# Kernel optimization log

Measured on AMD Instinct MI355X. Metric: run time of the kernel, lower is better.

## Reference

```python
import jax, jax.numpy as jnp
import numpy as np

N_NODES = 100000
N_EDGES = 1600000
F_IN = 128
HIDDEN = 64
N_CLASSES = 32


def setup_inputs() -> dict:
    key = jax.random.key(0)
    k1, k2, k3, k4 = jax.random.split(key, 4)
    x = jax.random.normal(k1, (N_NODES, F_IN), dtype=jnp.float32)
    edge_index = jax.random.randint(k2, (2, N_EDGES), 0, N_NODES, dtype=jnp.int32)
    # Glorot-style init for the two GCNConv weight matrices
    W1 = jax.random.normal(k3, (F_IN, HIDDEN), dtype=jnp.float32) * (1.0 / np.sqrt(F_IN))
    W2 = jax.random.normal(k4, (HIDDEN, N_CLASSES), dtype=jnp.float32) * (1.0 / np.sqrt(HIDDEN))
    b1 = jnp.zeros((HIDDEN,), dtype=jnp.float32)
    b2 = jnp.zeros((N_CLASSES,), dtype=jnp.float32)
    return {"x": x, "edge_index": edge_index, "W1": W1, "b1": b1, "W2": W2, "b2": b2}


def gcn_conv(x, W, b, src, dst, num_nodes):
    # PyG GCNConv: linear transform first, then normalized neighbor aggregation.
    h = x @ W  # [N, out]
    ones = jnp.ones(src.shape, dtype=h.dtype)
    deg = jax.ops.segment_sum(ones, dst, num_segments=num_nodes)  # in-degree incl. self-loops
    d_inv_sqrt = jnp.where(deg > 0, jax.lax.rsqrt(deg), 0.0)
    norm = d_inv_sqrt[src] * d_inv_sqrt[dst]  # [E]
    msg = h[src] * norm[:, None]              # gather + scale, [E, out]
    out = jax.ops.segment_sum(msg, dst, num_segments=num_nodes)  # scatter-add
    return out + b


def reference(x, edge_index, W1, b1, W2, b2):
    n = x.shape[0]
    # add_self_loops=True (GCNConv default)
    loop = jnp.arange(n, dtype=edge_index.dtype)
    src = jnp.concatenate([edge_index[0], loop])
    dst = jnp.concatenate([edge_index[1], loop])
    h = jax.nn.relu(gcn_conv(x, W1, b1, src, dst, n))
    # F.dropout(training=self.training) is identity in eval mode
    logits = gcn_conv(h, W2, b2, src, dst, n)
    return jax.nn.log_softmax(logits, axis=1)
```

## Files before the change

### kernel.cpp

```cpp
#include <hip/hip_runtime.h>

#define F_IN 128
#define HID 64
#define CLS 32
#define BCAP 8192

typedef short v8s __attribute__((ext_vector_type(8)));
typedef float f4 __attribute__((ext_vector_type(4)));
typedef float f2 __attribute__((ext_vector_type(2)));

__device__ __forceinline__ float bflo(unsigned int w) { return __uint_as_float(w << 16); }
__device__ __forceinline__ float bfhi(unsigned int w) { return __uint_as_float(w & 0xFFFF0000u); }
__device__ __forceinline__ unsigned short f2bf(float f) {
    unsigned int u = __float_as_uint(f);
    u += 0x7FFFu + ((u >> 16) & 1u);
    return (unsigned short)(u >> 16);
}
__device__ __forceinline__ unsigned int pack2(float lo, float hi) {
    return (unsigned int)f2bf(lo) | ((unsigned int)f2bf(hi) << 16);
}
__device__ __forceinline__ unsigned int relu2(unsigned int w) {
    unsigned int lo = (w & 0x8000u) ? 0u : (w & 0xFFFFu);
    unsigned int hi = (w & 0x80000000u) ? 0u : (w & 0xFFFF0000u);
    return lo | hi;
}
__device__ __forceinline__ unsigned char f2fp8(float v) {
    return (unsigned char)(__builtin_amdgcn_cvt_pk_fp8_f32(v, v, 0, false) & 0xFF);
}

__global__ __launch_bounds__(512) void k_init(int* __restrict__ bCursor, int nb) {
    int i = threadIdx.x;
    if (i < nb) bCursor[i] = i * BCAP;
}

__global__ __launch_bounds__(256) void k_bscatter(const int* __restrict__ src,
                                                  const int* __restrict__ dst,
                                                  int* __restrict__ bCursor,
                                                  int* __restrict__ bucketed, int E, int nb) {
    __shared__ int h[512];
    __shared__ int chunk[512];
    int tid = threadIdx.x;
    for (int i = tid; i < nb; i += 256) h[i] = 0;
    __syncthreads();

    int e0 = blockIdx.x * 2048;
    int myRec[8], myB[8], myRank[8];
#pragma unroll
    for (int k = 0; k < 8; ++k) {
        int e = e0 + k * 256 + tid;
        if (e < E) {
            int d = dst[e];
            myB[k] = d >> 8;
            myRec[k] = src[e] | ((d & 255) << 17);
            myRank[k] = atomicAdd(&h[myB[k]], 1);
        } else {
            myB[k] = -1;
        }
    }
    __syncthreads();
    for (int i = tid; i < nb; i += 256)
        chunk[i] = h[i] ? atomicAdd(&bCursor[i], h[i]) : 0;
    __syncthreads();
#pragma unroll
    for (int k = 0; k < 8; ++k) {
        if (myB[k] >= 0) bucketed[chunk[myB[k]] + myRank[k]] = myRec[k];
    }
}

__global__ __launch_bounds__(512) void k_csr(const int* __restrict__ bCursor,
                                             const int* __restrict__ bucketed,
                                             int* __restrict__ pk,
                                             float* __restrict__ dinv, int* __restrict__ csr,
                                             int n) {
    __shared__ int cnt[256];
    __shared__ int s[256];
    __shared__ int cur[256];
    int b = blockIdx.x;
    int node0 = b << 8;
    int tid = threadIdx.x;
    if (tid < 256) cnt[tid] = 0;
    __syncthreads();
    int p0 = b * BCAP, p1 = bCursor[b];
    for (int p = p0 + tid; p < p1; p += 512) {
        int rec = bucketed[p];
        atomicAdd(&cnt[rec >> 17], 1);
    }
    __syncthreads();
    int v = 0;
    if (tid < 256) { v = cnt[tid]; s[tid] = v; }
    __syncthreads();
    for (int off = 1; off < 256; off <<= 1) {
        int t = (tid >= off && tid < 256) ? s[tid - off] : 0;
        __syncthreads();
        if (tid < 256) s[tid] += t;
        __syncthreads();
    }
    if (tid < 256) {
        int myoff = p0 + s[tid] - v;
        cur[tid] = myoff;
        int node = node0 + tid;
        if (node < n) {
            pk[node] = myoff | (v << 22);
            dinv[node] = rsqrtf((float)(v + 1));
        }
    }
    __syncthreads();
    for (int p = p0 + tid; p < p1; p += 512) {
        int rec = bucketed[p];
        int q = atomicAdd(&cur[rec >> 17], 1);
        csr[q] = rec & 0x1FFFF;
    }
}

__global__ __launch_bounds__(256) void k_gemm1(const float* __restrict__ x,
                                               const float* __restrict__ W,
                                               const float* __restrict__ dinv,
                                               unsigned char* __restrict__ y, int n) {
    __shared__ unsigned short Wt[HID * 136];
    int tid = threadIdx.x;
    for (int i = tid; i < F_IN * HID; i += 256) {
        int k = i >> 6, nn = i & 63;
        Wt[nn * 136 + k] = f2bf(W[i]);
    }
    __syncthreads();

    int lane = tid & 63;
    int quad = lane >> 4, c = lane & 15;
    int nstripes = (n + 15) >> 4;
    int stripe = blockIdx.x * 4 + (tid >> 6);
    if (stripe >= nstripes) return;
    int row0 = stripe << 4;

    f4 acc[4] = {};
    union { unsigned int u[4]; v8s v; } au;

#pragma unroll
    for (int ks = 0; ks < 4; ++ks) {
        int k0 = ks * 32 + quad * 8;
        int row = row0 + c;
        if (row >= n) row = n - 1;
        const float* xp = x + (size_t)row * F_IN + k0;
        float4 lo = *(const float4*)xp;
        float4 hi = *(const float4*)(xp + 4);
        au.u[0] = pack2(lo.x, lo.y);
        au.u[1] = pack2(lo.z, lo.w);
        au.u[2] = pack2(hi.x, hi.y);
        au.u[3] = pack2(hi.z, hi.w);
        v8s a = au.v;
#pragma unroll
        for (int nt = 0; nt < 4; ++nt) {
            v8s b = *(const v8s*)&Wt[(nt * 16 + c) * 136 + k0];
            acc[nt] = __builtin_amdgcn_mfma_f32_16x16x32_bf16(a, b, acc[nt], 0, 0, 0);
        }
    }

#pragma unroll
    for (int reg = 0; reg < 4; ++reg) {
        int row = row0 + quad * 4 + reg;
        if (row < n) {
            float dd = dinv[row];
#pragma unroll
            for (int nt = 0; nt < 4; ++nt)
                y[(size_t)row * HID + nt * 16 + c] = f2fp8(acc[nt][reg] * dd);
        }
    }
}

__global__ __launch_bounds__(256) void k_gemm2(const unsigned short* __restrict__ hb,
                                               const float* __restrict__ W,
                                               const float* __restrict__ dinv,
                                               unsigned short* __restrict__ y, int n) {
    __shared__ unsigned short Wt[CLS * 72];
    int tid = threadIdx.x;
    for (int i = tid; i < HID * CLS; i += 256) {
        int k = i >> 5, nn = i & 31;
        Wt[nn * 72 + k] = f2bf(W[i]);
    }
    __syncthreads();

    int lane = tid & 63;
    int quad = lane >> 4, c = lane & 15;
    int nstripes = (n + 15) >> 4;
    int stripe = blockIdx.x * 4 + (tid >> 6);
    if (stripe >= nstripes) return;
    int row0 = stripe << 4;

    f4 acc[2] = {};
    union { unsigned int u[4]; v8s v; } au;

#pragma unroll
    for (int ks = 0; ks < 2; ++ks) {
        int k0 = ks * 32 + quad * 8;
        int row = row0 + c;
        if (row >= n) row = n - 1;
        uint4 w = *(const uint4*)(hb + (size_t)row * HID + k0);
        au.u[0] = relu2(w.x);
        au.u[1] = relu2(w.y);
        au.u[2] = relu2(w.z);
        au.u[3] = relu2(w.w);
        v8s a = au.v;
#pragma unroll
        for (int nt = 0; nt < 2; ++nt) {
            v8s b = *(const v8s*)&Wt[(nt * 16 + c) * 72 + k0];
            acc[nt] = __builtin_amdgcn_mfma_f32_16x16x32_bf16(a, b, acc[nt], 0, 0, 0);
        }
    }

#pragma unroll
    for (int reg = 0; reg < 4; ++reg) {
        int row = row0 + quad * 4 + reg;
        if (row < n) {
            float dd = dinv[row];
#pragma unroll
            for (int nt = 0; nt < 2; ++nt)
                y[(size_t)row * CLS + nt * 16 + c] = f2bf(acc[nt][reg] * dd);
        }
    }
}

__global__ __launch_bounds__(256) void k_gather64(const int* __restrict__ pk,
                                                  const int* __restrict__ csr,
                                                  const unsigned char* __restrict__ xw8,
                                                  const float* __restrict__ b,
                                                  unsigned short* __restrict__ hb, int n) {
    int node = blockIdx.x * 16 + (threadIdx.x >> 4);
    if (node >= n) return;
    int l = threadIdx.x & 15;
    unsigned int pv = (unsigned int)pk[node];
    int p0 = pv & 0x3FFFFF;
    int cntv = (int)(pv >> 22);
    int p1 = p0 + cntv;
    float dd = rsqrtf((float)(cntv + 1));
    unsigned int sw = *(const unsigned int*)(xw8 + (size_t)node * HID + l * 4);

    f2 A0 = {0.f, 0.f}, A1 = A0, B0 = A0, B1 = A0, C0 = A0, C1 = A0, D0 = A0, D1 = A0;
    int p = p0;
    for (; p + 3 < p1; p += 4) {
        int s0 = csr[p], s1 = csr[p + 1], s2 = csr[p + 2], s3 = csr[p + 3];
        unsigned int w0 = *(const unsigned int*)(xw8 + (size_t)s0 * HID + l * 4);
        unsigned int w1 = *(const unsigned int*)(xw8 + (size_t)s1 * HID + l * 4);
        unsigned int w2 = *(const unsigned int*)(xw8 + (size_t)s2 * HID + l * 4);
        unsigned int w3 = *(const unsigned int*)(xw8 + (size_t)s3 * HID + l * 4);
        A0 += __builtin_amdgcn_cvt_pk_f32_fp8(w0, false);
        A1 += __builtin_amdgcn_cvt_pk_f32_fp8(w0, true);
        B0 += __builtin_amdgcn_cvt_pk_f32_fp8(w1, false);
        B1 += __builtin_amdgcn_cvt_pk_f32_fp8(w1, true);
        C0 += __builtin_amdgcn_cvt_pk_f32_fp8(w2, false);
        C1 += __builtin_amdgcn_cvt_pk_f32_fp8(w2, true);
        D0 += __builtin_amdgcn_cvt_pk_f32_fp8(w3, false);
        D1 += __builtin_amdgcn_cvt_pk_f32_fp8(w3, true);
    }
    for (; p < p1; ++p) {
        int s = csr[p];
        unsigned int w = *(const unsigned int*)(xw8 + (size_t)s * HID + l * 4);
        A0 += __builtin_amdgcn_cvt_pk_f32_fp8(w, false);
        A1 += __builtin_amdgcn_cvt_pk_f32_fp8(w, true);
    }
    A0 += B0; C0 += D0; A0 += C0;
    A1 += B1; C1 += D1; A1 += C1;

    A0 += __builtin_amdgcn_cvt_pk_f32_fp8(sw, false);
    A1 += __builtin_amdgcn_cvt_pk_f32_fp8(sw, true);
    float4 bb = *(const float4*)(b + l * 4);
    uint2 o;
    o.x = pack2(A0.x * dd + bb.x, A0.y * dd + bb.y);
    o.y = pack2(A1.x * dd + bb.z, A1.y * dd + bb.w);
    *(uint2*)(hb + (size_t)node * HID + l * 4) = o;
}

__global__ __launch_bounds__(256) void k_gather32_lsm(const int* __restrict__ pk,
                                                      const int* __restrict__ csr,
                                                      const unsigned short* __restrict__ hwb,
                                                      const float* __restrict__ b,
                                                      float* __restrict__ out, int n) {
    int node = blockIdx.x * 16 + (threadIdx.x >> 4);
    if (node >= n) return;
    int l = threadIdx.x & 15;
    unsigned int pv = (unsigned int)pk[node];
    int p0 = pv & 0x3FFFFF;
    int cntv = (int)(pv >> 22);
    int p1 = p0 + cntv;
    float dd = rsqrtf((float)(cntv + 1));
    unsigned int sw = *(const unsigned int*)(hwb + (size_t)node * CLS + l * 2);

    float A0 = 0.f, A1 = 0.f, B0 = 0.f, B1 = 0.f, C0 = 0.f, C1 = 0.f, D0 = 0.f, D1 = 0.f;
    int p = p0;
    for (; p + 3 < p1; p += 4) {
        int s0 = csr[p], s1 = csr[p + 1], s2 = csr[p + 2], s3 = csr[p + 3];
        unsigned int w0 = *(const unsigned int*)(hwb + (size_t)s0 * CLS + l * 2);
        unsigned int w1 = *(const unsigned int*)(hwb + (size_t)s1 * CLS + l * 2);
        unsigned int w2 = *(const unsigned int*)(hwb + (size_t)s2 * CLS + l * 2);
        unsigned int w3 = *(const unsigned int*)(hwb + (size_t)s3 * CLS + l * 2);
        A0 += bflo(w0); A1 += bfhi(w0);
        B0 += bflo(w1); B1 += bfhi(w1);
        C0 += bflo(w2); C1 += bfhi(w2);
        D0 += bflo(w3); D1 += bfhi(w3);
    }
    for (; p < p1; ++p) {
        int s = csr[p];
        unsigned int w = *(const unsigned int*)(hwb + (size_t)s * CLS + l * 2);
        A0 += bflo(w); A1 += bfhi(w);
    }
    A0 += B0; C0 += D0; A0 += C0;
    A1 += B1; C1 += D1; A1 += C1;

    float v0 = (A0 + bflo(sw)) * dd + b[l * 2];
    float v1 = (A1 + bfhi(sw)) * dd + b[l * 2 + 1];

    float m = fmaxf(v0, v1);
    m = fmaxf(m, __shfl_xor(m, 1));
    m = fmaxf(m, __shfl_xor(m, 2));
    m = fmaxf(m, __shfl_xor(m, 4));
    m = fmaxf(m, __shfl_xor(m, 8));
    float s = __expf(v0 - m) + __expf(v1 - m);
    s += __shfl_xor(s, 1);
    s += __shfl_xor(s, 2);
    s += __shfl_xor(s, 4);
    s += __shfl_xor(s, 8);
    float ls = m + __logf(s);
    float2 o;
    o.x = v0 - ls;
    o.y = v1 - ls;
    *(float2*)(out + (size_t)node * CLS + l * 2) = o;
}

extern "C" void kernel_launch(void* const* d_in, const int* in_sizes, int n_in,
                              void* d_out, int out_size, void* d_ws, size_t ws_size,
                              hipStream_t stream) {
    const float* x  = (const float*)d_in[0];
    const int* edge = (const int*)d_in[1];
    const float* W1 = (const float*)d_in[2];
    const float* b1 = (const float*)d_in[3];
    const float* W2 = (const float*)d_in[4];
    const float* b2 = (const float*)d_in[5];
    float* out = (float*)d_out;

    int N = in_sizes[0] / F_IN;
    int E = in_sizes[1] / 2;
    const int* src = edge;
    const int* dst = edge + E;
    int NB = (N + 255) >> 8;

    float* dinv    = (float*)d_ws;
    int* pk        = (int*)(dinv + N);
    int* bCursor   = pk + N;
    int* csr       = bCursor + 512;
    int* bucketed  = csr + (size_t)NB * BCAP;
    unsigned char* bufA = (unsigned char*)(bucketed + (size_t)NB * BCAP);
    unsigned short* bufB = (unsigned short*)(bufA + (size_t)N * HID);

    k_init<<<1, 512, 0, stream>>>(bCursor, NB);
    k_bscatter<<<(E + 2047) / 2048, 256, 0, stream>>>(src, dst, bCursor, bucketed, E, NB);
    k_csr<<<NB, 512, 0, stream>>>(bCursor, bucketed, pk, dinv, csr, N);

    int nstripes16 = (N + 15) >> 4;
    int gemmBlocks = (nstripes16 + 3) / 4;
    int gatherBlocks = (N + 15) / 16;

    k_gemm1<<<gemmBlocks, 256, 0, stream>>>(x, W1, dinv, bufA, N);
    k_gather64<<<gatherBlocks, 256, 0, stream>>>(pk, csr, bufA, b1, bufB, N);

    k_gemm2<<<gemmBlocks, 256, 0, stream>>>(bufB, W2, dinv, (unsigned short*)bufA, N);
    k_gather32_lsm<<<gatherBlocks, 256, 0, stream>>>(pk, csr, (unsigned short*)bufA, b2, out, N);
}
```

Before: 216.5 us.

## Fuse layer-1 aggregation with second GEMM, widen gather lanes, single-pass CSR build

The layer-1 neighbor aggregation now runs in the same kernel as the W2 GEMM. Each block gathers 32 nodes into shared memory as ReLU'd bf16 and runs MFMA there, so the intermediate hidden buffer no longer goes through global memory and one launch is dropped. The layer-2 gather now uses 4 lanes per node with 16-byte loads instead of 16 lanes with 4-byte loads, which cuts the number of index loads and shuffle steps. The CSR build keeps the bucketed records and their ranks in registers, so it no longer rereads the buckets or does a second round of shared atomics. The costs are fewer threads per node, which gives less memory parallelism per row, and extra register pressure from the 16-entry per-thread arrays.

```diff
diff --git a/kernel.cpp b/kernel.cpp
--- a/kernel.cpp
+++ b/kernel.cpp
@@ -18,11 +18,6 @@
 }
 __device__ __forceinline__ unsigned int pack2(float lo, float hi) {
     return (unsigned int)f2bf(lo) | ((unsigned int)f2bf(hi) << 16);
-}
-__device__ __forceinline__ unsigned int relu2(unsigned int w) {
-    unsigned int lo = (w & 0x8000u) ? 0u : (w & 0xFFFFu);
-    unsigned int hi = (w & 0x80000000u) ? 0u : (w & 0xFFFF0000u);
-    return lo | hi;
 }
 __device__ __forceinline__ unsigned char f2fp8(float v) {
     return (unsigned char)(__builtin_amdgcn_cvt_pk_fp8_f32(v, v, 0, false) & 0xFF);
@@ -74,16 +69,25 @@
                                              int n) {
     __shared__ int cnt[256];
     __shared__ int s[256];
-    __shared__ int cur[256];
+    __shared__ int baseS[256];
     int b = blockIdx.x;
     int node0 = b << 8;
     int tid = threadIdx.x;
     if (tid < 256) cnt[tid] = 0;
     __syncthreads();
     int p0 = b * BCAP, p1 = bCursor[b];
-    for (int p = p0 + tid; p < p1; p += 512) {
-        int rec = bucketed[p];
-        atomicAdd(&cnt[rec >> 17], 1);
+
+    int rec[16], rnk[16];
+#pragma unroll
+    for (int k = 0; k < 16; ++k) {
+        int p = p0 + tid + (k << 9);
+        if (p < p1) {
+            int r = bucketed[p];
+            rec[k] = r;
+            rnk[k] = atomicAdd(&cnt[r >> 17], 1);
+        } else {
+            rec[k] = -1;
+        }
     }
     __syncthreads();
     int v = 0;
@@ -97,7 +101,7 @@
     }
     if (tid < 256) {
         int myoff = p0 + s[tid] - v;
-        cur[tid] = myoff;
+        baseS[tid] = myoff;
         int node = node0 + tid;
         if (node < n) {
             pk[node] = myoff | (v << 22);
@@ -105,10 +109,9 @@
         }
     }
     __syncthreads();
-    for (int p = p0 + tid; p < p1; p += 512) {
-        int rec = bucketed[p];
-        int q = atomicAdd(&cur[rec >> 17], 1);
-        csr[q] = rec & 0x1FFFF;
+#pragma unroll
+    for (int k = 0; k < 16; ++k) {
+        if (rec[k] >= 0) csr[baseS[rec[k] >> 17] + rnk[k]] = rec[k] & 0x1FFFF;
     }
 }
 
@@ -149,8 +152,8 @@
         v8s a = au.v;
 #pragma unroll
         for (int nt = 0; nt < 4; ++nt) {
-            v8s b = *(const v8s*)&Wt[(nt * 16 + c) * 136 + k0];
-            acc[nt] = __builtin_amdgcn_mfma_f32_16x16x32_bf16(a, b, acc[nt], 0, 0, 0);
+            v8s bb = *(const v8s*)&Wt[(nt * 16 + c) * 136 + k0];
+            acc[nt] = __builtin_amdgcn_mfma_f32_16x16x32_bf16(a, bb, acc[nt], 0, 0, 0);
         }
     }
 
@@ -166,162 +169,183 @@
     }
 }
 
-__global__ __launch_bounds__(256) void k_gemm2(const unsigned short* __restrict__ hb,
-                                               const float* __restrict__ W,
-                                               const float* __restrict__ dinv,
-                                               unsigned short* __restrict__ y, int n) {
+__global__ __launch_bounds__(256) void k_gather64_w2(const int* __restrict__ pk,
+                                                     const int* __restrict__ csr,
+                                                     const unsigned char* __restrict__ xw8,
+                                                     const float* __restrict__ b1,
+                                                     const float* __restrict__ W2,
+                                                     const float* __restrict__ dinv,
+                                                     unsigned short* __restrict__ y2, int n) {
     __shared__ unsigned short Wt[CLS * 72];
+    __shared__ unsigned short Hl[32 * 72];
     int tid = threadIdx.x;
     for (int i = tid; i < HID * CLS; i += 256) {
         int k = i >> 5, nn = i & 31;
-        Wt[nn * 72 + k] = f2bf(W[i]);
-    }
-    __syncthreads();
-
-    int lane = tid & 63;
-    int quad = lane >> 4, c = lane & 15;
-    int nstripes = (n + 15) >> 4;
-    int stripe = blockIdx.x * 4 + (tid >> 6);
-    if (stripe >= nstripes) return;
-    int row0 = stripe << 4;
-
-    f4 acc[2] = {};
-    union { unsigned int u[4]; v8s v; } au;
-
+        Wt[nn * 72 + k] = f2bf(W2[i]);
+    }
+
+    int g = tid >> 3;
+    int l = tid & 7;
+    int node = blockIdx.x * 32 + g;
+    bool alive = node < n;
+
+    if (alive) {
+        unsigned int pv = (unsigned int)pk[node];
+        int p0 = pv & 0x3FFFFF;
+        int cntv = (int)(pv >> 22);
+        int p1 = p0 + cntv;
+        float dd = rsqrtf((float)(cntv + 1));
+        uint2 sw = *(const uint2*)(xw8 + (size_t)node * HID + l * 8);
+
+        f2 a0 = {0.f, 0.f}, a1 = a0, a2 = a0, a3 = a0;
+        f2 c0 = a0, c1 = a0, c2 = a0, c3 = a0;
+        int p = p0;
+        for (; p + 3 < p1; p += 4) {
+            int s0 = csr[p], s1 = csr[p + 1], s2 = csr[p + 2], s3 = csr[p + 3];
+            uint2 w0 = *(const uint2*)(xw8 + (size_t)s0 * HID + l * 8);
+            uint2 w1 = *(const uint2*)(xw8 + (size_t)s1 * HID + l * 8);
+            uint2 w2 = *(const uint2*)(xw8 + (size_t)s2 * HID + l * 8);
+            uint2 w3 = *(const uint2*)(xw8 + (size_t)s3 * HID + l * 8);
+            a0 += __builtin_amdgcn_cvt_pk_f32_fp8(w0.x, false);
+            a1 += __builtin_amdgcn_cvt_pk_f32_fp8(w0.x, true);
+            a2 += __builtin_amdgcn_cvt_pk_f32_fp8(w0.y, false);
+            a3 += __builtin_amdgcn_cvt_pk_f32_fp8(w0.y, true);
+            c0 += __builtin_amdgcn_cvt_pk_f32_fp8(w1.x, false);
+            c1 += __builtin_amdgcn_cvt_pk_f32_fp8(w1.x, true);
+            c2 += __builtin_amdgcn_cvt_pk_f32_fp8(w1.y, false);
+            c3 += __builtin_amdgcn_cvt_pk_f32_fp8(w1.y, true);
+            a0 += __builtin_amdgcn_cvt_pk_f32_fp8(w2.x, false);
+            a1 += __builtin_amdgcn_cvt_pk_f32_fp8(w2.x, true);
+            a2 += __builtin_amdgcn_cvt_pk_f32_fp8(w2.y, false);
+            a3 += __builtin_amdgcn_cvt_pk_f32_fp8(w2.y, true);
+            c0 += __builtin_amdgcn_cvt_pk_f32_fp8(w3.x, false);
+            c1 += __builtin_amdgcn_cvt_pk_f32_fp8(w3.x, true);
+            c2 += __builtin_amdgcn_cvt_pk_f32_fp8(w3.y, false);
+            c3 += __builtin_amdgcn_cvt_pk_f32_fp8(w3.y, true);
+        }
+        for (; p < p1; ++p) {
+            int s0 = csr[p];
+            uint2 w0 = *(const uint2*)(xw8 + (size_t)s0 * HID + l * 8);
+            a0 += __builtin_amdgcn_cvt_pk_f32_fp8(w0.x, false);
+            a1 += __builtin_amdgcn_cvt_pk_f32_fp8(w0.x, true);
+            a2 += __builtin_amdgcn_cvt_pk_f32_fp8(w0.y, false);
+            a3 += __builtin_amdgcn_cvt_pk_f32_fp8(w0.y, true);
+        }
+        a0 += c0; a1 += c1; a2 += c2; a3 += c3;
+        a0 += __builtin_amdgcn_cvt_pk_f32_fp8(sw.x, false);
+        a1 += __builtin_amdgcn_cvt_pk_f32_fp8(sw.x, true);
+        a2 += __builtin_amdgcn_cvt_pk_f32_fp8(sw.y, false);
+        a3 += __builtin_amdgcn_cvt_pk_f32_fp8(sw.y, true);
+
+        float4 bb0 = *(const float4*)(b1 + l * 8);
+        float4 bb1 = *(const float4*)(b1 + l * 8 + 4);
+        float h0 = fmaxf(a0.x * dd + bb0.x, 0.f);
+        float h1 = fmaxf(a0.y * dd + bb0.y, 0.f);
+        float h2 = fmaxf(a1.x * dd + bb0.z, 0.f);
+        float h3 = fmaxf(a1.y * dd + bb0.w, 0.f);
+        float h4 = fmaxf(a2.x * dd + bb1.x, 0.f);
+        float h5 = fmaxf(a2.y * dd + bb1.y, 0.f);
+        float h6 = fmaxf(a3.x * dd + bb1.z, 0.f);
+        float h7 = fmaxf(a3.y * dd + bb1.w, 0.f);
+        uint4 hp;
+        hp.x = pack2(h0, h1);
+        hp.y = pack2(h2, h3);
+        hp.z = pack2(h4, h5);
+        hp.w = pack2(h6, h7);
+        *(uint4*)&Hl[g * 72 + l * 8] = hp;
+    }
+    __syncthreads();
+
+    int wv = tid >> 6;
+    int t = wv & 1, nt = wv >> 1;
+    int lane = tid & 63, quad = lane >> 4, c = lane & 15;
+    f4 acc = {};
 #pragma unroll
     for (int ks = 0; ks < 2; ++ks) {
         int k0 = ks * 32 + quad * 8;
-        int row = row0 + c;
-        if (row >= n) row = n - 1;
-        uint4 w = *(const uint4*)(hb + (size_t)row * HID + k0);
-        au.u[0] = relu2(w.x);
-        au.u[1] = relu2(w.y);
-        au.u[2] = relu2(w.z);
-        au.u[3] = relu2(w.w);
-        v8s a = au.v;
-#pragma unroll
-        for (int nt = 0; nt < 2; ++nt) {
-            v8s b = *(const v8s*)&Wt[(nt * 16 + c) * 72 + k0];
-            acc[nt] = __builtin_amdgcn_mfma_f32_16x16x32_bf16(a, b, acc[nt], 0, 0, 0);
-        }
-    }
-
+        v8s aF = *(const v8s*)&Hl[(t * 16 + c) * 72 + k0];
+        v8s bF = *(const v8s*)&Wt[(nt * 16 + c) * 72 + k0];
+        acc = __builtin_amdgcn_mfma_f32_16x16x32_bf16(aF, bF, acc, 0, 0, 0);
+    }
+    int row0 = blockIdx.x * 32 + t * 16;
 #pragma unroll
     for (int reg = 0; reg < 4; ++reg) {
         int row = row0 + quad * 4 + reg;
         if (row < n) {
-            float dd = dinv[row];
-#pragma unroll
-            for (int nt = 0; nt < 2; ++nt)
-                y[(size_t)row * CLS + nt * 16 + c] = f2bf(acc[nt][reg] * dd);
-        }
-    }
-}
-
-__global__ __launch_bounds__(256) void k_gather64(const int* __restrict__ pk,
-                                                  const int* __restrict__ csr,
-                                                  const unsigned char* __restrict__ xw8,
-                                                  const float* __restrict__ b,
-                                                  unsigned short* __restrict__ hb, int n) {
-    int node = blockIdx.x * 16 + (threadIdx.x >> 4);
+            float dd2 = dinv[row];
+            y2[(size_t)row * CLS + nt * 16 + c] = f2bf(acc[reg] * dd2);
+        }
+    }
+}
+
+__global__ __launch_bounds__(256) void k_gather32_lsm(const int* __restrict__ pk,
+                                                      const int* __restrict__ csr,
+                                                      const unsigned short* __restrict__ hwb,
+                                                      const float* __restrict__ b,
+                                                      float* __restrict__ out, int n) {
+    int tid = threadIdx.x;
+    int node = blockIdx.x * 64 + (tid >> 2);
     if (node >= n) return;
-    int l = threadIdx.x & 15;
+    int l = tid & 3;
     unsigned int pv = (unsigned int)pk[node];
     int p0 = pv & 0x3FFFFF;
     int cntv = (int)(pv >> 22);
     int p1 = p0 + cntv;
     float dd = rsqrtf((float)(cntv + 1));
-    unsigned int sw = *(const unsigned int*)(xw8 + (size_t)node * HID + l * 4);
-
-    f2 A0 = {0.f, 0.f}, A1 = A0, B0 = A0, B1 = A0, C0 = A0, C1 = A0, D0 = A0, D1 = A0;
+    uint4 sw = *(const uint4*)(hwb + (size_t)node * CLS + l * 8);
+
+    float A0 = 0.f, A1 = 0.f, A2 = 0.f, A3 = 0.f, A4 = 0.f, A5 = 0.f, A6 = 0.f, A7 = 0.f;
+    float B0 = 0.f, B1 = 0.f, B2 = 0.f, B3 = 0.f, B4 = 0.f, B5 = 0.f, B6 = 0.f, B7 = 0.f;
     int p = p0;
     for (; p + 3 < p1; p += 4) {
         int s0 = csr[p], s1 = csr[p + 1], s2 = csr[p + 2], s3 = csr[p + 3];
-        unsigned int w0 = *(const unsigned int*)(xw8 + (size_t)s0 * HID + l * 4);
-        unsigned int w1 = *(const unsigned int*)(xw8 + (size_t)s1 * HID + l * 4);
-        unsigned int w2 = *(const unsigned int*)(xw8 + (size_t)s2 * HID + l * 4);
-        unsigned int w3 = *(const unsigned int*)(xw8 + (size_t)s3 * HID + l * 4);
-        A0 += __builtin_amdgcn_cvt_pk_f32_fp8(w0, false);
-        A1 += __builtin_amdgcn_cvt_pk_f32_fp8(w0, true);
-        B0 += __builtin_amdgcn_cvt_pk_f32_fp8(w1, false);
-        B1 += __builtin_amdgcn_cvt_pk_f32_fp8(w1, true);
-        C0 += __builtin_amdgcn_cvt_pk_f32_fp8(w2, false);
-        C1 += __builtin_amdgcn_cvt_pk_f32_fp8(w2, true);
-        D0 += __builtin_amdgcn_cvt_pk_f32_fp8(w3, false);
-        D1 += __builtin_amdgcn_cvt_pk_f32_fp8(w3, true);
+        uint4 w0 = *(const uint4*)(hwb + (size_t)s0 * CLS + l * 8);
+        uint4 w1 = *(const uint4*)(hwb + (size_t)s1 * CLS + l * 8);
+        uint4 w2 = *(const uint4*)(hwb + (size_t)s2 * CLS + l * 8);
+        uint4 w3 = *(const uint4*)(hwb + (size_t)s3 * CLS + l * 8);
+        A0 += bflo(w0.x); A1 += bfhi(w0.x); A2 += bflo(w0.y); A3 += bfhi(w0.y);
+        A4 += bflo(w0.z); A5 += bfhi(w0.z); A6 += bflo(w0.w); A7 += bfhi(w0.w);
+        B0 += bflo(w1.x); B1 += bfhi(w1.x); B2 += bflo(w1.y); B3 += bfhi(w1.y);
+        B4 += bflo(w1.z); B5 += bfhi(w1.z); B6 += bflo(w1.w); B7 += bfhi(w1.w);
+        A0 += bflo(w2.x); A1 += bfhi(w2.x); A2 += bflo(w2.y); A3 += bfhi(w2.y);
+        A4 += bflo(w2.z); A5 += bfhi(w2.z); A6 += bflo(w2.w); A7 += bfhi(w2.w);
+        B0 += bflo(w3.x); B1 += bfhi(w3.x); B2 += bflo(w3.y); B3 += bfhi(w3.y);
+        B4 += bflo(w3.z); B5 += bfhi(w3.z); B6 += bflo(w3.w); B7 += bfhi(w3.w);
     }
     for (; p < p1; ++p) {
-        int s = csr[p];
-        unsigned int w = *(const unsigned int*)(xw8 + (size_t)s * HID + l * 4);
-        A0 += __builtin_amdgcn_cvt_pk_f32_fp8(w, false);
-        A1 += __builtin_amdgcn_cvt_pk_f32_fp8(w, true);
-    }
-    A0 += B0; C0 += D0; A0 += C0;
-    A1 += B1; C1 += D1; A1 += C1;
-
-    A0 += __builtin_amdgcn_cvt_pk_f32_fp8(sw, false);
-    A1 += __builtin_amdgcn_cvt_pk_f32_fp8(sw, true);
-    float4 bb = *(const float4*)(b + l * 4);
-    uint2 o;
-    o.x = pack2(A0.x * dd + bb.x, A0.y * dd + bb.y);
-    o.y = pack2(A1.x * dd + bb.z, A1.y * dd + bb.w);
-    *(uint2*)(hb + (size_t)node * HID + l * 4) = o;
-}
-
-__global__ __launch_bounds__(256) void k_gather32_lsm(const int* __restrict__ pk,
-                                                      const int* __restrict__ csr,
-                                                      const unsigned short* __restrict__ hwb,
-                                                      const float* __restrict__ b,
-                                                      float* __restrict__ out, int n) {
-    int node = blockIdx.x * 16 + (threadIdx.x >> 4);
-    if (node >= n) return;
-    int l = threadIdx.x & 15;
-    unsigned int pv = (unsigned int)pk[node];
-    int p0 = pv & 0x3FFFFF;
-    int cntv = (int)(pv >> 22);
-    int p1 = p0 + cntv;
-    float dd = rsqrtf((float)(cntv + 1));
-    unsigned int sw = *(const unsigned int*)(hwb + (size_t)node * CLS + l * 2);
-
-    float A0 = 0.f, A1 = 0.f, B0 = 0.f, B1 = 0.f, C0 = 0.f, C1 = 0.f, D0 = 0.f, D1 = 0.f;
-    int p = p0;
-    for (; p + 3 < p1; p += 4) {
-        int s0 = csr[p], s1 = csr[p + 1], s2 = csr[p + 2], s3 = csr[p + 3];
-        unsigned int w0 = *(const unsigned int*)(hwb + (size_t)s0 * CLS + l * 2);
-        unsigned int w1 = *(const unsigned int*)(hwb + (size_t)s1 * CLS + l * 2);
-        unsigned int w2 = *(const unsigned int*)(hwb + (size_t)s2 * CLS + l * 2);
-        unsigned int w3 = *(const unsigned int*)(hwb + (size_t)s3 * CLS + l * 2);
-        A0 += bflo(w0); A1 += bfhi(w0);
-        B0 += bflo(w1); B1 += bfhi(w1);
-        C0 += bflo(w2); C1 += bfhi(w2);
-        D0 += bflo(w3); D1 += bfhi(w3);
-    }
-    for (; p < p1; ++p) {
-        int s = csr[p];
-        unsigned int w = *(const unsigned int*)(hwb + (size_t)s * CLS + l * 2);
-        A0 += bflo(w); A1 += bfhi(w);
-    }
-    A0 += B0; C0 += D0; A0 += C0;
-    A1 += B1; C1 += D1; A1 += C1;
-
-    float v0 = (A0 + bflo(sw)) * dd + b[l * 2];
-    float v1 = (A1 + bfhi(sw)) * dd + b[l * 2 + 1];
-
-    float m = fmaxf(v0, v1);
+        int s0 = csr[p];
+        uint4 w0 = *(const uint4*)(hwb + (size_t)s0 * CLS + l * 8);
+        A0 += bflo(w0.x); A1 += bfhi(w0.x); A2 += bflo(w0.y); A3 += bfhi(w0.y);
+        A4 += bflo(w0.z); A5 += bfhi(w0.z); A6 += bflo(w0.w); A7 += bfhi(w0.w);
+    }
+    A0 += B0; A1 += B1; A2 += B2; A3 += B3;
+    A4 += B4; A5 += B5; A6 += B6; A7 += B7;
+
+    float4 bb0 = *(const float4*)(b + l * 8);
+    float4 bb1 = *(const float4*)(b + l * 8 + 4);
+    float v0 = (A0 + bflo(sw.x)) * dd + bb0.x;
+    float v1 = (A1 + bfhi(sw.x)) * dd + bb0.y;
+    float v2 = (A2 + bflo(sw.y)) * dd + bb0.z;
+    float v3 = (A3 + bfhi(sw.y)) * dd + bb0.w;
+    float v4 = (A4 + bflo(sw.z)) * dd + bb1.x;
+    float v5 = (A5 + bfhi(sw.z)) * dd + bb1.y;
+    float v6 = (A6 + bflo(sw.w)) * dd + bb1.z;
+    float v7 = (A7 + bfhi(sw.w)) * dd + bb1.w;
+
+    float m = fmaxf(fmaxf(fmaxf(v0, v1), fmaxf(v2, v3)), fmaxf(fmaxf(v4, v5), fmaxf(v6, v7)));
     m = fmaxf(m, __shfl_xor(m, 1));
     m = fmaxf(m, __shfl_xor(m, 2));
-    m = fmaxf(m, __shfl_xor(m, 4));
-    m = fmaxf(m, __shfl_xor(m, 8));
-    float s = __expf(v0 - m) + __expf(v1 - m);
+    float s = __expf(v0 - m) + __expf(v1 - m) + __expf(v2 - m) + __expf(v3 - m) +
+              __expf(v4 - m) + __expf(v5 - m) + __expf(v6 - m) + __expf(v7 - m);
     s += __shfl_xor(s, 1);
     s += __shfl_xor(s, 2);
-    s += __shfl_xor(s, 4);
-    s += __shfl_xor(s, 8);
     float ls = m + __logf(s);
-    float2 o;
-    o.x = v0 - ls;
-    o.y = v1 - ls;
-    *(float2*)(out + (size_t)node * CLS + l * 2) = o;
+    float4 o0, o1;
+    o0.x = v0 - ls; o0.y = v1 - ls; o0.z = v2 - ls; o0.w = v3 - ls;
+    o1.x = v4 - ls; o1.y = v5 - ls; o1.z = v6 - ls; o1.w = v7 - ls;
+    float* op = out + (size_t)node * CLS + l * 8;
+    *(float4*)op = o0;
+    *(float4*)(op + 4) = o1;
 }
 
 extern "C" void kernel_launch(void* const* d_in, const int* in_sizes, int n_in,
@@ -347,7 +371,7 @@
     int* csr       = bCursor + 512;
     int* bucketed  = csr + (size_t)NB * BCAP;
     unsigned char* bufA = (unsigned char*)(bucketed + (size_t)NB * BCAP);
-    unsigned short* bufB = (unsigned short*)(bufA + (size_t)N * HID);
+    unsigned short* y2  = (unsigned short*)(bufA + (size_t)N * HID);
 
     k_init<<<1, 512, 0, stream>>>(bCursor, NB);
     k_bscatter<<<(E + 2047) / 2048, 256, 0, stream>>>(src, dst, bCursor, bucketed, E, NB);
@@ -355,11 +379,10 @@
 
     int nstripes16 = (N + 15) >> 4;
     int gemmBlocks = (nstripes16 + 3) / 4;
-    int gatherBlocks = (N + 15) / 16;
 
     k_gemm1<<<gemmBlocks, 256, 0, stream>>>(x, W1, dinv, bufA, N);
-    k_gather64<<<gatherBlocks, 256, 0, stream>>>(pk, csr, bufA, b1, bufB, N);
-
-    k_gemm2<<<gemmBlocks, 256, 0, stream>>>(bufB, W2, dinv, (unsigned short*)bufA, N);
-    k_gather32_lsm<<<gatherBlocks, 256, 0, stream>>>(pk, csr, (unsigned short*)bufA, b2, out, N);
-}
+
+    k_gather64_w2<<<(N + 31) / 32, 256, 0, stream>>>(pk, csr, bufA, b1, W2, dinv, y2, N);
+
+    k_gather32_lsm<<<(N + 63) / 64, 256, 0, stream>>>(pk, csr, y2, b2, out, N);
+}
```

Result: faster. 203.0 us (-6.3%).
